# Kernel tuning notes

Hardware: AMD Instinct MI355X
Metric: run time of the kernel (lower is better)

Reference implementation:

```python
import jax, jax.numpy as jnp
import numpy as np

B, T, N, M, D = 4, 64, 32, 32, 128  # batch, time, price points, liquidity points, feature dim


def setup_inputs() -> dict:
    key = jax.random.key(0)
    ks = jax.random.split(key, 6)
    w = lambda k, shape: jax.random.normal(k, shape, jnp.float32) * 0.05
    return {
        "price": jax.random.normal(ks[0], (B, T, N, D), jnp.float32),
        "liquid": jax.random.normal(ks[1], (B, T, M, D), jnp.float32),
        "W_p": w(ks[2], (D, D)), "b_p": jnp.zeros((D,), jnp.float32),
        "W_v": w(ks[3], (D, D)), "b_v": jnp.zeros((D,), jnp.float32),
        "W1": w(ks[4], (4 * D, D)), "b1": jnp.zeros((D,), jnp.float32),
        "W2": w(ks[5], (D, D)), "b2": jnp.zeros((D,), jnp.float32),
    }


def reference(price, liquid, W_p, b_p, W_v, b_v, W1, b1, W2, b2):
    # proj_p / proj_v
    p = price @ W_p + b_p    # [B, T, N, D]
    v = liquid @ W_v + b_v   # [B, T, M, D]
    p4 = p[:, :, :, None, :]  # [B, T, N, 1, D]
    v4 = v[:, :, None, :, :]  # [B, T, 1, M, D]
    prod = p4 * v4            # [B, T, N, M, D]
    absdiff = jnp.abs(p4 - v4)
    full = (p.shape[0], p.shape[1], p.shape[2], v.shape[2], p.shape[3])
    pair = jnp.concatenate(
        [jnp.broadcast_to(p4, full), jnp.broadcast_to(v4, full), prod, absdiff],
        axis=-1,
    )  # [B, T, N, M, 4D]
    h = jax.nn.silu(pair @ W1 + b1)  # [B, T, N, M, D]
    grid = h @ W2 + b2               # [B, T, N, M, D]
    return grid.reshape(grid.shape[0], grid.shape[1], grid.shape[2] * grid.shape[3], grid.shape[4])
```

## Files before the change

### kernel.cpp

```cpp
#include <hip/hip_runtime.h>


typedef short  short8  __attribute__((ext_vector_type(8)));
typedef float  f32x4   __attribute__((ext_vector_type(4)));
typedef float  f32x16  __attribute__((ext_vector_type(16)));

#define DEV static __device__ __forceinline__

DEV float bf2f(unsigned short h) {
  unsigned u = ((unsigned)h) << 16;
  float f;
  __builtin_memcpy(&f, &u, 4);
  return f;
}
DEV unsigned short f2bf(float f) {
  unsigned u;
  __builtin_memcpy(&u, &f, 4);
  unsigned r = (u + 0x7FFFu + ((u >> 16) & 1u)) >> 16;
  return (unsigned short)r;
}

__global__ void k0_prep(const float* __restrict__ Wp, const float* __restrict__ bp,
                        const float* __restrict__ Wv, const float* __restrict__ bv,
                        const float* __restrict__ W1, const float* __restrict__ b1,
                        const float* __restrict__ W2,
                        unsigned short* __restrict__ w1cd, unsigned short* __restrict__ w2sw,
                        unsigned short* __restrict__ wpsw, unsigned short* __restrict__ gpsw,
                        unsigned short* __restrict__ wvsw, unsigned short* __restrict__ gvsw,
                        float* __restrict__ c1) {
  int t = blockIdx.x * 256 + threadIdx.x;
  if (t < 32768) {
    int j = t & 7, lane = (t >> 3) & 63, r2 = t >> 9;
    int ct = r2 & 3, kt = r2 >> 2;
    int k = kt * 16 + (lane >> 5) * 8 + j;
    int c = ct * 32 + (lane & 31);
    w1cd[t] = f2bf(W1[(256 + k) * 128 + c]);
  } else if (t < 114688) {
    int e = t - 32768;
    int sec = e >> 14;
    int f = e & 16383;
    int j = f & 7, lane = (f >> 3) & 63, r2 = f >> 9;
    int kt = r2 & 3, ct = r2 >> 2;
    int k = kt * 32 + ((lane >> 4) & 3) * 8 + j;
    int n = ct * 16 + (lane & 15);
    if (sec == 0) {
      w2sw[f] = f2bf(W2[k * 128 + n]);
    } else if (sec == 1) {
      wpsw[f] = f2bf(Wp[k * 128 + n]);
    } else if (sec == 2) {
      float s = 0.f;
      for (int e2 = 0; e2 < 128; e2++) s += Wp[k * 128 + e2] * W1[e2 * 128 + n];
      gpsw[f] = f2bf(s);
    } else if (sec == 3) {
      wvsw[f] = f2bf(Wv[k * 128 + n]);
    } else {
      float s = 0.f;
      for (int e2 = 0; e2 < 128; e2++) s += Wv[k * 128 + e2] * W1[(128 + e2) * 128 + n];
      gvsw[f] = f2bf(s);
    }
  } else if (t < 114816) {
    int c = t - 114688;
    float s = b1[c];
    for (int e2 = 0; e2 < 128; e2++)
      s += bp[e2] * W1[e2 * 128 + c] + bv[e2] * W1[(128 + e2) * 128 + c];
    c1[c] = s;
  }
}

__global__ __launch_bounds__(256, 2) void k1_proj(
    const float* __restrict__ price, const float* __restrict__ liquid,
    const float* __restrict__ bp, const float* __restrict__ bv, const float* __restrict__ c1,
    const unsigned short* __restrict__ wpsw, const unsigned short* __restrict__ gpsw,
    const unsigned short* __restrict__ wvsw, const unsigned short* __restrict__ gvsw,
    unsigned short* __restrict__ pbf, unsigned short* __restrict__ vbf,
    float* __restrict__ pAc, unsigned short* __restrict__ vbsw) {
  __shared__ __align__(16) unsigned short sA[128 * 136];
  int b = blockIdx.x;
  int chunk = b >> 2, sel = b & 3;
  int side = sel >> 1, half = sel & 1;
  int rowbase = chunk * 128;
  const float* src = side ? liquid : price;
  const unsigned short* bsw = side ? (half ? gvsw : wvsw) : (half ? gpsw : wpsw);
  int tid = threadIdx.x;

#pragma unroll
  for (int i = 0; i < 16; i++) {
    int e4 = i * 256 + tid;
    int row = e4 >> 5, c4 = (e4 & 31) * 4;
    float4 f = *(const float4*)(src + (rowbase + row) * 128 + c4);
    unsigned u0 = (unsigned)f2bf(f.x) | ((unsigned)f2bf(f.y) << 16);
    unsigned u1 = (unsigned)f2bf(f.z) | ((unsigned)f2bf(f.w) << 16);
    uint2 pk; pk.x = u0; pk.y = u1;
    *(uint2*)&sA[row * 136 + c4] = pk;
  }
  __syncthreads();

  int lane = tid & 63, w = tid >> 6;
  int l15 = lane & 15, q4 = lane >> 4;
  f32x4 acc[2][8] = {};
#pragma unroll
  for (int kt = 0; kt < 4; kt++) {
    short8 a0 = *(const short8*)&sA[(w * 32 + l15) * 136 + kt * 32 + q4 * 8];
    short8 a1 = *(const short8*)&sA[(w * 32 + 16 + l15) * 136 + kt * 32 + q4 * 8];
#pragma unroll
    for (int ct = 0; ct < 8; ct++) {
      short8 bfr = *(const short8*)(bsw + ((ct * 4 + kt) * 64 + lane) * 8);
      acc[0][ct] = __builtin_amdgcn_mfma_f32_16x16x32_bf16(a0, bfr, acc[0][ct], 0, 0, 0);
      acc[1][ct] = __builtin_amdgcn_mfma_f32_16x16x32_bf16(a1, bfr, acc[1][ct], 0, 0, 0);
    }
  }

#pragma unroll
  for (int rg = 0; rg < 2; rg++) {
#pragma unroll
    for (int ct = 0; ct < 8; ct++) {
      int col = ct * 16 + l15;
      int lrow0 = w * 32 + rg * 16 + q4 * 4;
#pragma unroll
      for (int ri = 0; ri < 4; ri++) {
        int grow = rowbase + lrow0 + ri;
        float val = acc[rg][ct][ri];
        if (side == 0) {
          if (half == 0) pbf[grow * 128 + col] = f2bf(val + bp[col]);
          else           pAc[grow * 128 + col] = val + c1[col];
        } else {
          if (half == 0) vbf[grow * 128 + col] = f2bf(val + bv[col]);
          else {
            int btl = grow >> 5, m = grow & 31;
            int idx = btl * 4096 +
                      ((((m >> 4) * 4 + (col >> 5)) * 64) + ((m >> 3) & 1) * 32 + (col & 31)) * 8 +
                      (m & 7);
            vbsw[idx] = f2bf(val);
          }
        }
      }
    }
  }
}

__global__ __launch_bounds__(256, 2) void k2_pair(
    const unsigned short* __restrict__ pbf, const unsigned short* __restrict__ vbf,
    const float* __restrict__ pAc, const unsigned short* __restrict__ w1cd,
    const unsigned short* __restrict__ vbsw, unsigned short* __restrict__ hsw) {
  __shared__ __align__(16) unsigned short sVf[4096];
  __shared__ __align__(16) unsigned short sP[8 * 136];
  __shared__ float sPA[8 * 128];
  __shared__ __align__(16) unsigned short sH[4][2][16 * 136];
  int bt = blockIdx.x >> 2, n0 = (blockIdx.x & 3) * 8;
  int tid = threadIdx.x;

  if (tid < 128) {
    int row = tid >> 4, seg = tid & 15;
    *(uint4*)&sP[row * 136 + seg * 8] = *(const uint4*)(pbf + (bt * 32 + n0 + row) * 128 + seg * 8);
  }
#pragma unroll
  for (int g2 = 0; g2 < 2; g2++) {
    int g = tid * 2 + g2;
    int m = g & 31, k0 = (g >> 5) * 8;
    *(uint4*)&sVf[g * 8] = *(const uint4*)(vbf + (bt * 32 + m) * 128 + k0);
  }
  {
    int row = tid >> 5, c4 = (tid & 31) * 4;
    *(float4*)&sPA[row * 128 + c4] = *(const float4*)(pAc + (bt * 32 + n0 + row) * 128 + c4);
  }
  __syncthreads();

  int lane = tid & 63, w = tid >> 6;
  int m31 = lane & 31, hi = lane >> 5, l15 = lane & 15, q4 = lane >> 4;
  int na = 2 * w, nb = 2 * w + 1;
  const unsigned short* vbswt = vbsw + bt * 4096;

  f32x16 acc0[4] = {};
  f32x16 acc1[4] = {};

#pragma unroll
  for (int kt = 0; kt < 8; kt++) {
    short8 vf = *(const short8*)&sVf[((kt * 2 + hi) * 32 + m31) * 8];
    short8 p0 = *(const short8*)&sP[na * 136 + kt * 16 + hi * 8];
    short8 p1 = *(const short8*)&sP[nb * 136 + kt * 16 + hi * 8];
    short8 x0, y0, x1, y1;
#pragma unroll
    for (int j = 0; j < 8; j++) {
      float vv = bf2f((unsigned short)vf[j]);
      float a = bf2f((unsigned short)p0[j]);
      float c = bf2f((unsigned short)p1[j]);
      x0[j] = (short)f2bf(a * vv);
      y0[j] = (short)f2bf(fabsf(a - vv));
      x1[j] = (short)f2bf(c * vv);
      y1[j] = (short)f2bf(fabsf(c - vv));
    }
    const unsigned short* bxb = w1cd + (kt * 4) * 512;
    const unsigned short* byb = w1cd + ((kt + 8) * 4) * 512;
#pragma unroll
    for (int ct = 0; ct < 4; ct++) {
      short8 bx = *(const short8*)(bxb + ct * 512 + lane * 8);
      short8 by = *(const short8*)(byb + ct * 512 + lane * 8);
      acc0[ct] = __builtin_amdgcn_mfma_f32_32x32x16_bf16(x0, bx, acc0[ct], 0, 0, 0);
      acc1[ct] = __builtin_amdgcn_mfma_f32_32x32x16_bf16(x1, bx, acc1[ct], 0, 0, 0);
      acc0[ct] = __builtin_amdgcn_mfma_f32_32x32x16_bf16(y0, by, acc0[ct], 0, 0, 0);
      acc1[ct] = __builtin_amdgcn_mfma_f32_32x32x16_bf16(y1, by, acc1[ct], 0, 0, 0);
    }
  }

#pragma unroll
  for (int kt2 = 0; kt2 < 2; kt2++) {
    short8 indf;
#pragma unroll
    for (int j = 0; j < 8; j++)
      indf[j] = (short)(((kt2 * 16 + hi * 8 + j) == m31) ? 0x3F80 : 0);
#pragma unroll
    for (int ct = 0; ct < 4; ct++) {
      short8 bi = *(const short8*)(vbswt + (kt2 * 4 + ct) * 512 + lane * 8);
      acc0[ct] = __builtin_amdgcn_mfma_f32_32x32x16_bf16(indf, bi, acc0[ct], 0, 0, 0);
      acc1[ct] = __builtin_amdgcn_mfma_f32_32x32x16_bf16(indf, bi, acc1[ct], 0, 0, 0);
    }
  }

#pragma unroll
  for (int ct = 0; ct < 4; ct++) {
    float t0 = sPA[na * 128 + ct * 32 + m31];
    float t1 = sPA[nb * 128 + ct * 32 + m31];
#pragma unroll
    for (int i = 0; i < 16; i++) { acc0[ct][i] += t0; acc1[ct][i] += t1; }
  }

  auto stage_store = [&](const f32x16* A, int nloc) {
#pragma unroll
    for (int ch = 0; ch < 2; ch++) {
      unsigned short* sHw = &sH[w][ch][0];
#pragma unroll
      for (int ct = 0; ct < 4; ct++) {
#pragma unroll
        for (int r8 = 0; r8 < 8; r8++) {
          int reg = ch * 8 + r8;
          float z = A[ct][reg];
          float hv = z / (1.f + __expf(-z));
          int row16 = (reg & 3) + 8 * ((reg >> 2) & 1) + 4 * hi;
          sHw[row16 * 136 + ct * 32 + m31] = f2bf(hv);
        }
      }
      int rg = bt * 64 + nloc * 2 + ch;
#pragma unroll
      for (int kt2 = 0; kt2 < 4; kt2++) {
        uint4 fr = *(const uint4*)&sHw[l15 * 136 + kt2 * 32 + q4 * 8];
        *(uint4*)(hsw + ((rg * 4 + kt2) * 64 + lane) * 8) = fr;
      }
    }
  };
  stage_store(acc0, n0 + na);
  stage_store(acc1, n0 + nb);
}

__global__ __launch_bounds__(256, 2) void k3_out(
    const unsigned short* __restrict__ hsw, const unsigned short* __restrict__ w2sw,
    const float* __restrict__ b2, float* __restrict__ out) {
  __shared__ __align__(16) unsigned short sW2[16384];
  __shared__ float sB2[128];
  int tid = threadIdx.x;
#pragma unroll
  for (int i = 0; i < 8; i++) {
    int e = i * 256 + tid;
    *(uint4*)&sW2[e * 8] = *(const uint4*)(w2sw + e * 8);
  }
  if (tid < 128) sB2[tid] = b2[tid];
  __syncthreads();

  int lane = tid & 63, w = tid >> 6;
  int l15 = lane & 15, q4 = lane >> 4;
  int rg0 = blockIdx.x * 16 + w * 4;

  f32x4 acc[4][8] = {};
#pragma unroll
  for (int kt = 0; kt < 4; kt++) {
    short8 hf[4];
#pragma unroll
    for (int rgi = 0; rgi < 4; rgi++)
      hf[rgi] = *(const short8*)(hsw + (((rg0 + rgi) * 4 + kt) * 64 + lane) * 8);
#pragma unroll
    for (int ct = 0; ct < 8; ct++) {
      short8 bfr = *(const short8*)&sW2[((ct * 4 + kt) * 64 + lane) * 8];
#pragma unroll
      for (int rgi = 0; rgi < 4; rgi++)
        acc[rgi][ct] = __builtin_amdgcn_mfma_f32_16x16x32_bf16(hf[rgi], bfr, acc[rgi][ct], 0, 0, 0);
    }
  }
#pragma unroll
  for (int rgi = 0; rgi < 4; rgi++) {
    int growb = (rg0 + rgi) * 16 + q4 * 4;
#pragma unroll
    for (int ct = 0; ct < 8; ct++) {
      int col = ct * 16 + l15;
      float bias = sB2[col];
#pragma unroll
      for (int ri = 0; ri < 4; ri++)
        out[(growb + ri) * 128 + col] = acc[rgi][ct][ri] + bias;
    }
  }
}

extern "C" void kernel_launch(void* const* d_in, const int* in_sizes, int n_in,
                              void* d_out, int out_size, void* d_ws, size_t ws_size,
                              hipStream_t stream) {
  const float* price  = (const float*)d_in[0];
  const float* liquid = (const float*)d_in[1];
  const float* Wp     = (const float*)d_in[2];
  const float* bp     = (const float*)d_in[3];
  const float* Wv     = (const float*)d_in[4];
  const float* bv     = (const float*)d_in[5];
  const float* W1     = (const float*)d_in[6];
  const float* b1     = (const float*)d_in[7];
  const float* W2     = (const float*)d_in[8];
  const float* b2     = (const float*)d_in[9];

  char* ws = (char*)d_ws;
  unsigned short* w1cd = (unsigned short*)(ws + 0);
  unsigned short* w2sw = (unsigned short*)(ws + 65536);
  unsigned short* wpsw = (unsigned short*)(ws + 98304);
  unsigned short* gpsw = (unsigned short*)(ws + 131072);
  unsigned short* wvsw = (unsigned short*)(ws + 163840);
  unsigned short* gvsw = (unsigned short*)(ws + 196608);
  float*          c1   = (float*)(ws + 229376);
  unsigned short* pbf  = (unsigned short*)(ws + 262144);
  unsigned short* vbf  = (unsigned short*)(ws + 2359296);
  float*          pAc  = (float*)(ws + 4456448);
  unsigned short* vbsw = (unsigned short*)(ws + 8650752);
  unsigned short* hsw  = (unsigned short*)(ws + 10747904);

  hipLaunchKernelGGL(k0_prep, dim3(449), dim3(256), 0, stream,
                     Wp, bp, Wv, bv, W1, b1, W2, w1cd, w2sw, wpsw, gpsw, wvsw, gvsw, c1);
  hipLaunchKernelGGL(k1_proj, dim3(256), dim3(256), 0, stream,
                     price, liquid, bp, bv, c1, wpsw, gpsw, wvsw, gvsw, pbf, vbf, pAc, vbsw);
  hipLaunchKernelGGL(k2_pair, dim3(1024), dim3(256), 0, stream,
                     pbf, vbf, pAc, w1cd, vbsw, hsw);
  hipLaunchKernelGGL(k3_out, dim3(1024), dim3(256), 0, stream,
                     hsw, w2sw, b2, (float*)d_out);
}
```

Baseline: 242.8 us.

## Fuse pair-MLP first layer with W2 output GEMM in one kernel

Merges the k2 pair kernel and the k3 output kernel so the SiLU activations go through LDS into 32x32 MFMAs against W2 inside the same wave. This removes the round trip of the bf16 hidden tensor through global memory and one kernel launch. W2 is relaid out in k0 to match the 32x32 fragment layout and is read directly from global/L2 per wave rather than staged in LDS. pAc and b2 are now loaded into registers instead of shared memory, which raises register pressure.

```diff
diff --git a/kernel.cpp b/kernel.cpp
--- a/kernel.cpp
+++ b/kernel.cpp
@@ -40,23 +40,28 @@
     int sec = e >> 14;
     int f = e & 16383;
     int j = f & 7, lane = (f >> 3) & 63, r2 = f >> 9;
-    int kt = r2 & 3, ct = r2 >> 2;
-    int k = kt * 32 + ((lane >> 4) & 3) * 8 + j;
-    int n = ct * 16 + (lane & 15);
     if (sec == 0) {
-      w2sw[f] = f2bf(W2[k * 128 + n]);
-    } else if (sec == 1) {
-      wpsw[f] = f2bf(Wp[k * 128 + n]);
-    } else if (sec == 2) {
-      float s = 0.f;
-      for (int e2 = 0; e2 < 128; e2++) s += Wp[k * 128 + e2] * W1[e2 * 128 + n];
-      gpsw[f] = f2bf(s);
-    } else if (sec == 3) {
-      wvsw[f] = f2bf(Wv[k * 128 + n]);
+      int ct = r2 & 3, kt = r2 >> 2;
+      int k = kt * 16 + (lane >> 5) * 8 + j;
+      int c = ct * 32 + (lane & 31);
+      w2sw[f] = f2bf(W2[k * 128 + c]);
     } else {
-      float s = 0.f;
-      for (int e2 = 0; e2 < 128; e2++) s += Wv[k * 128 + e2] * W1[(128 + e2) * 128 + n];
-      gvsw[f] = f2bf(s);
+      int kt = r2 & 3, ct = r2 >> 2;
+      int k = kt * 32 + ((lane >> 4) & 3) * 8 + j;
+      int n = ct * 16 + (lane & 15);
+      if (sec == 1) {
+        wpsw[f] = f2bf(Wp[k * 128 + n]);
+      } else if (sec == 2) {
+        float s = 0.f;
+        for (int e2 = 0; e2 < 128; e2++) s += Wp[k * 128 + e2] * W1[e2 * 128 + n];
+        gpsw[f] = f2bf(s);
+      } else if (sec == 3) {
+        wvsw[f] = f2bf(Wv[k * 128 + n]);
+      } else {
+        float s = 0.f;
+        for (int e2 = 0; e2 < 128; e2++) s += Wv[k * 128 + e2] * W1[(128 + e2) * 128 + n];
+        gvsw[f] = f2bf(s);
+      }
     }
   } else if (t < 114816) {
     int c = t - 114688;
@@ -138,14 +143,14 @@
   }
 }
 
-__global__ __launch_bounds__(256, 2) void k2_pair(
+__global__ __launch_bounds__(256, 2) void k2_fused(
     const unsigned short* __restrict__ pbf, const unsigned short* __restrict__ vbf,
     const float* __restrict__ pAc, const unsigned short* __restrict__ w1cd,
-    const unsigned short* __restrict__ vbsw, unsigned short* __restrict__ hsw) {
+    const unsigned short* __restrict__ vbsw, const unsigned short* __restrict__ w2sw,
+    const float* __restrict__ b2, float* __restrict__ out) {
   __shared__ __align__(16) unsigned short sVf[4096];
   __shared__ __align__(16) unsigned short sP[8 * 136];
-  __shared__ float sPA[8 * 128];
-  __shared__ __align__(16) unsigned short sH[4][2][16 * 136];
+  __shared__ __align__(16) unsigned short sHt[4][32 * 136];
   int bt = blockIdx.x >> 2, n0 = (blockIdx.x & 3) * 8;
   int tid = threadIdx.x;
 
@@ -159,16 +164,20 @@
     int m = g & 31, k0 = (g >> 5) * 8;
     *(uint4*)&sVf[g * 8] = *(const uint4*)(vbf + (bt * 32 + m) * 128 + k0);
   }
-  {
-    int row = tid >> 5, c4 = (tid & 31) * 4;
-    *(float4*)&sPA[row * 128 + c4] = *(const float4*)(pAc + (bt * 32 + n0 + row) * 128 + c4);
-  }
   __syncthreads();
 
   int lane = tid & 63, w = tid >> 6;
-  int m31 = lane & 31, hi = lane >> 5, l15 = lane & 15, q4 = lane >> 4;
+  int m31 = lane & 31, hi = lane >> 5;
   int na = 2 * w, nb = 2 * w + 1;
   const unsigned short* vbswt = vbsw + bt * 4096;
+
+  float pa0[4], pa1[4], bia[4];
+#pragma unroll
+  for (int ct = 0; ct < 4; ct++) {
+    pa0[ct] = pAc[(bt * 32 + n0 + na) * 128 + ct * 32 + m31];
+    pa1[ct] = pAc[(bt * 32 + n0 + nb) * 128 + ct * 32 + m31];
+    bia[ct] = b2[ct * 32 + m31];
+  }
 
   f32x16 acc0[4] = {};
   f32x16 acc1[4] = {};
@@ -218,84 +227,47 @@
 
 #pragma unroll
   for (int ct = 0; ct < 4; ct++) {
-    float t0 = sPA[na * 128 + ct * 32 + m31];
-    float t1 = sPA[nb * 128 + ct * 32 + m31];
-#pragma unroll
-    for (int i = 0; i < 16; i++) { acc0[ct][i] += t0; acc1[ct][i] += t1; }
-  }
-
-  auto stage_store = [&](const f32x16* A, int nloc) {
-#pragma unroll
-    for (int ch = 0; ch < 2; ch++) {
-      unsigned short* sHw = &sH[w][ch][0];
+#pragma unroll
+    for (int i = 0; i < 16; i++) { acc0[ct][i] += pa0[ct]; acc1[ct][i] += pa1[ct]; }
+  }
+
+  unsigned short* sh = &sHt[w][0];
+  auto tail = [&](const f32x16* A, int n) {
+#pragma unroll
+    for (int ct = 0; ct < 4; ct++) {
+#pragma unroll
+      for (int reg = 0; reg < 16; reg++) {
+        float z = A[ct][reg];
+        float hv = z / (1.f + __expf(-z));
+        int mr = (reg & 3) + 8 * (reg >> 2) + 4 * hi;
+        sh[mr * 136 + ct * 32 + m31] = f2bf(hv);
+      }
+    }
+    short8 hf[8];
+#pragma unroll
+    for (int kt = 0; kt < 8; kt++)
+      hf[kt] = *(const short8*)&sh[m31 * 136 + kt * 16 + hi * 8];
+    f32x16 o[4] = {};
+#pragma unroll
+    for (int kt = 0; kt < 8; kt++) {
 #pragma unroll
       for (int ct = 0; ct < 4; ct++) {
-#pragma unroll
-        for (int r8 = 0; r8 < 8; r8++) {
-          int reg = ch * 8 + r8;
-          float z = A[ct][reg];
-          float hv = z / (1.f + __expf(-z));
-          int row16 = (reg & 3) + 8 * ((reg >> 2) & 1) + 4 * hi;
-          sHw[row16 * 136 + ct * 32 + m31] = f2bf(hv);
-        }
-      }
-      int rg = bt * 64 + nloc * 2 + ch;
-#pragma unroll
-      for (int kt2 = 0; kt2 < 4; kt2++) {
-        uint4 fr = *(const uint4*)&sHw[l15 * 136 + kt2 * 32 + q4 * 8];
-        *(uint4*)(hsw + ((rg * 4 + kt2) * 64 + lane) * 8) = fr;
+        short8 wf = *(const short8*)(w2sw + ((kt * 4 + ct) * 64 + lane) * 8);
+        o[ct] = __builtin_amdgcn_mfma_f32_32x32x16_bf16(hf[kt], wf, o[ct], 0, 0, 0);
+      }
+    }
+    int rowb = bt * 1024 + n * 32;
+#pragma unroll
+    for (int ct = 0; ct < 4; ct++) {
+#pragma unroll
+      for (int reg = 0; reg < 16; reg++) {
+        int mr = (reg & 3) + 8 * (reg >> 2) + 4 * hi;
+        out[(rowb + mr) * 128 + ct * 32 + m31] = o[ct][reg] + bia[ct];
       }
     }
   };
-  stage_store(acc0, n0 + na);
-  stage_store(acc1, n0 + nb);
-}
-
-__global__ __launch_bounds__(256, 2) void k3_out(
-    const unsigned short* __restrict__ hsw, const unsigned short* __restrict__ w2sw,
-    const float* __restrict__ b2, float* __restrict__ out) {
-  __shared__ __align__(16) unsigned short sW2[16384];
-  __shared__ float sB2[128];
-  int tid = threadIdx.x;
-#pragma unroll
-  for (int i = 0; i < 8; i++) {
-    int e = i * 256 + tid;
-    *(uint4*)&sW2[e * 8] = *(const uint4*)(w2sw + e * 8);
-  }
-  if (tid < 128) sB2[tid] = b2[tid];
-  __syncthreads();
-
-  int lane = tid & 63, w = tid >> 6;
-  int l15 = lane & 15, q4 = lane >> 4;
-  int rg0 = blockIdx.x * 16 + w * 4;
-
-  f32x4 acc[4][8] = {};
-#pragma unroll
-  for (int kt = 0; kt < 4; kt++) {
-    short8 hf[4];
-#pragma unroll
-    for (int rgi = 0; rgi < 4; rgi++)
-      hf[rgi] = *(const short8*)(hsw + (((rg0 + rgi) * 4 + kt) * 64 + lane) * 8);
-#pragma unroll
-    for (int ct = 0; ct < 8; ct++) {
-      short8 bfr = *(const short8*)&sW2[((ct * 4 + kt) * 64 + lane) * 8];
-#pragma unroll
-      for (int rgi = 0; rgi < 4; rgi++)
-        acc[rgi][ct] = __builtin_amdgcn_mfma_f32_16x16x32_bf16(hf[rgi], bfr, acc[rgi][ct], 0, 0, 0);
-    }
-  }
-#pragma unroll
-  for (int rgi = 0; rgi < 4; rgi++) {
-    int growb = (rg0 + rgi) * 16 + q4 * 4;
-#pragma unroll
-    for (int ct = 0; ct < 8; ct++) {
-      int col = ct * 16 + l15;
-      float bias = sB2[col];
-#pragma unroll
-      for (int ri = 0; ri < 4; ri++)
-        out[(growb + ri) * 128 + col] = acc[rgi][ct][ri] + bias;
-    }
-  }
+  tail(acc0, n0 + na);
+  tail(acc1, n0 + nb);
 }
 
 extern "C" void kernel_launch(void* const* d_in, const int* in_sizes, int n_in,
@@ -324,14 +296,11 @@
   unsigned short* vbf  = (unsigned short*)(ws + 2359296);
   float*          pAc  = (float*)(ws + 4456448);
   unsigned short* vbsw = (unsigned short*)(ws + 8650752);
-  unsigned short* hsw  = (unsigned short*)(ws + 10747904);
 
   hipLaunchKernelGGL(k0_prep, dim3(449), dim3(256), 0, stream,
                      Wp, bp, Wv, bv, W1, b1, W2, w1cd, w2sw, wpsw, gpsw, wvsw, gvsw, c1);
   hipLaunchKernelGGL(k1_proj, dim3(256), dim3(256), 0, stream,
                      price, liquid, bp, bv, c1, wpsw, gpsw, wvsw, gvsw, pbf, vbf, pAc, vbsw);
-  hipLaunchKernelGGL(k2_pair, dim3(1024), dim3(256), 0, stream,
-                     pbf, vbf, pAc, w1cd, vbsw, hsw);
-  hipLaunchKernelGGL(k3_out, dim3(1024), dim3(256), 0, stream,
-                     hsw, w2sw, b2, (float*)d_out);
-}
+  hipLaunchKernelGGL(k2_fused, dim3(1024), dim3(256), 0, stream,
+                     pbf, vbf, pAc, w1cd, vbsw, w2sw, b2, (float*)d_out);
+}
```

After: 242.8 us. About the same (-0.0%).
